# Optimization experiments

Measured on AMD Instinct MI355X. Metric: run time of the kernel, lower is better.

Reference implementation:

```python
import jax, jax.numpy as jnp
import numpy as np

N_HEADS = 16
HEAD = 64
HID = 1024
WIN = 256
LN_EPS = 1e-5


def _ln(x, g, b):
    m = jnp.mean(x, axis=-1, keepdims=True)
    v = jnp.mean((x - m) ** 2, axis=-1, keepdims=True)
    return (x - m) * jax.lax.rsqrt(v + LN_EPS) * g + b


def _window_shift(x):
    return jnp.concatenate([jnp.zeros_like(x[:, :WIN]), x[:, :-WIN]], axis=1)


def _additive_attn(x, vec, mask_add):
    B, S, _ = x.shape
    # per-head logits: (x * vec) summed within each head, scaled
    attn = (x * vec).reshape(B, S, N_HEADS, HEAD).sum(-1) / (HEAD ** 0.5)
    attn = jnp.exp(attn + mask_add)[..., None]          # [B,S,H,1]
    xh = x.reshape(B, S, N_HEADS, HEAD)
    s = jnp.cumsum(attn * xh, axis=1)
    s = s - _window_shift(s)                             # windowed cumsum of attn*x
    z = jnp.cumsum(attn, axis=1)
    z = z - _window_shift(z)                             # windowed cumsum of attn
    return (s / z).reshape(B, S, HID)


def setup_inputs():
    key = jax.random.key(0)
    ks = jax.random.split(key, 7)
    B, S = 4, 4096
    w = lambda k: (jax.random.normal(k, (HID, HID)) * 0.02).astype(jnp.float32)
    return {
        "hidden_states": jax.random.normal(ks[0], (B, S, HID), dtype=jnp.float32),
        "attention_mask": jnp.ones((B, S), dtype=jnp.float32),
        "Wq": w(ks[1]), "Wk": w(ks[2]), "Wv": w(ks[3]), "Wp": w(ks[4]),
        "query_attn": (jax.random.normal(ks[5], (HID,)) * 0.02).astype(jnp.float32),
        "key_attn": (jax.random.normal(ks[6], (HID,)) * 0.02).astype(jnp.float32),
        "ln1_g": jnp.ones((HID,), jnp.float32), "ln1_b": jnp.zeros((HID,), jnp.float32),
        "ln2_g": jnp.ones((HID,), jnp.float32), "ln2_b": jnp.zeros((HID,), jnp.float32),
    }


def reference(hidden_states, attention_mask, Wq, Wk, Wv, Wp, query_attn, key_attn,
              ln1_g, ln1_b, ln2_g, ln2_b):
    h = _ln(hidden_states, ln1_g, ln1_b)
    query = h @ Wq.T
    keys = h @ Wk.T
    values = h @ Wv.T
    mask_add = ((1.0 - attention_mask) * -10000.0)[:, :, None]  # [B,S,1]
    pooled_q = _additive_attn(query, query_attn, mask_add)
    pooled_q = pooled_q @ Wp.T                                  # (dropout is identity in eval)
    residual = h + pooled_q * keys
    mixed = _ln(residual, ln2_g, ln2_b)
    pooled_k = _additive_attn(mixed, key_attn, mask_add)
    return residual + pooled_k * values
```

## Files before the change

### kernel.cpp

```cpp
#include <hip/hip_runtime.h>
#include <hip/hip_bf16.h>

#define HID 1024
#define NH 16
#define HEAD 64
#define WIN 256
#define SEQ 4096
#define BATCH 4
#define NROWS (BATCH * SEQ)
#define LN_EPS 1e-5f

typedef unsigned short u16;
typedef __bf16 bf16x8 __attribute__((ext_vector_type(8)));
typedef float f32x4 __attribute__((ext_vector_type(4)));

static __device__ inline float bfu(u16 u) {
    union { unsigned int i; float f; } x;
    x.i = ((unsigned int)u) << 16;
    return x.f;
}

static __device__ inline u16 f2bf(float f) {
    union { float f; unsigned int i; } x;
    x.f = f;
    unsigned int lsb = (x.i >> 16) & 1u;
    x.i += 0x7fffu + lsb;
    return (u16)(x.i >> 16);
}

__global__ __launch_bounds__(256) void ln1_conv(
    const float* __restrict__ x, const float* __restrict__ g,
    const float* __restrict__ b, u16* __restrict__ out,
    const float* __restrict__ wq, const float* __restrict__ wk,
    const float* __restrict__ wv, const float* __restrict__ wp,
    u16* __restrict__ wo)
{
    __shared__ float red[8];
    int t = threadIdx.x;
    if (blockIdx.x >= NROWS) {
        int i = (blockIdx.x - NROWS) * 256 + t;
        const int n = 1024 * 1024;
        wo[i]         = f2bf(wq[i]);
        wo[n + i]     = f2bf(wk[i]);
        wo[2 * n + i] = f2bf(wv[i]);
        wo[3 * n + i] = f2bf(wp[i]);
        return;
    }
    int row = blockIdx.x;
    float4 v = ((const float4*)(x + (size_t)row * HID))[t];
    float s  = v.x + v.y + v.z + v.w;
    float ss = v.x * v.x + v.y * v.y + v.z * v.z + v.w * v.w;
    #pragma unroll
    for (int off = 32; off; off >>= 1) { s += __shfl_down(s, off); ss += __shfl_down(ss, off); }
    int wave = t >> 6, lane = t & 63;
    if (lane == 0) { red[wave] = s; red[4 + wave] = ss; }
    __syncthreads();
    float S  = red[0] + red[1] + red[2] + red[3];
    float SS = red[4] + red[5] + red[6] + red[7];
    float mean = S * (1.f / HID);
    float var  = SS * (1.f / HID) - mean * mean;
    float inv  = rsqrtf(var + LN_EPS);
    float4 gv = ((const float4*)g)[t];
    float4 bv = ((const float4*)b)[t];
    ushort4 o;
    o.x = f2bf((v.x - mean) * inv * gv.x + bv.x);
    o.y = f2bf((v.y - mean) * inv * gv.y + bv.y);
    o.z = f2bf((v.z - mean) * inv * gv.z + bv.z);
    o.w = f2bf((v.w - mean) * inv * gv.w + bv.w);
    ((ushort4*)(out + (size_t)row * HID))[t] = o;
}

#define GLDS(gp, lp) __builtin_amdgcn_global_load_lds( \
    (const __attribute__((address_space(1))) void*)(gp), \
    (__attribute__((address_space(3))) void*)(lp), 16, 0, 0)

__global__ __launch_bounds__(512, 2) void gemm256(
    const u16* __restrict__ A, const u16* __restrict__ W,
    u16* __restrict__ C, int K, int ldc, int ntiles)
{
    __shared__ __align__(16) u16 sA[2][256 * 64];
    __shared__ __align__(16) u16 sB[2][256 * 64];

    const int tid = threadIdx.x;
    const int wave = tid >> 6, lane = tid & 63;
    const int wr = wave >> 2, wc = wave & 3;

    const int rp = tid >> 3;
    const int rowA = (rp < 32 ? rp : rp + 96);
    const int colE = (((tid & 7) * 16) ^ ((rp & 7) << 4)) >> 1;
    const int c0 = ((lane >> 4) * 16) ^ ((lane & 7) << 4);
    const int li = lane & 15;

    const int nk = K >> 6;

    int a = blockIdx.x;
    int wgl = a >> 3;
    int bm = (a & 7) * 8 + (wgl & 7);
    int bn = wgl >> 3;
    const u16* gA = A + (size_t)(bm * 256 + rowA) * K + colE;
    const u16* gB = W + (size_t)(bn * 256 + rp) * K + colE;
    #pragma unroll
    for (int w = 0; w < 4; ++w) GLDS(gB + (size_t)w * 64 * K, &sB[0][w * 4096 + tid * 8]);
    #pragma unroll
    for (int p = 0; p < 4; ++p) GLDS(gA + (size_t)p * 32 * K, &sA[0][p * 4096 + tid * 8]);

    while (true) {
        f32x4 acc[8][4];
        #pragma unroll
        for (int m = 0; m < 8; ++m)
            #pragma unroll
            for (int n = 0; n < 4; ++n) {
                f32x4 z = {0.f, 0.f, 0.f, 0.f};
                acc[m][n] = z;
            }

        for (int kt = 0; kt < nk; ++kt) {
            const int b = kt & 1;
            const u16* rA = sA[b];
            const u16* rB = sB[b];
            u16* dA = sA[b ^ 1];
            u16* dB = sB[b ^ 1];
            const bool pf = (kt + 1 < nk);

            if (pf) {
                const size_t ko = (size_t)(kt + 1) * 64;
                #pragma unroll
                for (int w = 0; w < 4; ++w)
                    GLDS(gB + (size_t)w * 64 * K + ko, &dB[w * 4096 + tid * 8]);
                #pragma unroll
                for (int p = 0; p < 4; ++p)
                    GLDS(gA + (size_t)p * 32 * K + ko, &dA[p * 4096 + tid * 8]);
                asm volatile("s_waitcnt vmcnt(8)" ::: "memory");
            } else {
                asm volatile("s_waitcnt vmcnt(0)" ::: "memory");
            }
            __builtin_amdgcn_sched_barrier(0);
            __builtin_amdgcn_s_barrier();
            __builtin_amdgcn_sched_barrier(0);

            bf16x8 bF0[4], bF1[4], aF0[8], aF1[8];
            #pragma unroll
            for (int n = 0; n < 4; ++n)
                bF0[n] = *(const bf16x8*)&rB[wc * 4096 + (n * 16 + li) * 64 + (c0 >> 1)];
            #pragma unroll
            for (int mf = 0; mf < 8; ++mf)
                aF0[mf] = *(const bf16x8*)&rA[(mf >> 1) * 4096 +
                    (wr * 32 + (mf & 1) * 16 + li) * 64 + (c0 >> 1)];
            __builtin_amdgcn_s_setprio(1);
            #pragma unroll
            for (int mf = 0; mf < 8; ++mf)
                #pragma unroll
                for (int n = 0; n < 4; ++n)
                    acc[mf][n] = __builtin_amdgcn_mfma_f32_16x16x32_bf16(
                        aF0[mf], bF0[n], acc[mf][n], 0, 0, 0);
            #pragma unroll
            for (int n = 0; n < 4; ++n)
                bF1[n] = *(const bf16x8*)&rB[wc * 4096 + (n * 16 + li) * 64 + ((c0 ^ 64) >> 1)];
            #pragma unroll
            for (int mf = 0; mf < 8; ++mf)
                aF1[mf] = *(const bf16x8*)&rA[(mf >> 1) * 4096 +
                    (wr * 32 + (mf & 1) * 16 + li) * 64 + ((c0 ^ 64) >> 1)];
            #pragma unroll
            for (int mf = 0; mf < 8; ++mf)
                #pragma unroll
                for (int n = 0; n < 4; ++n)
                    acc[mf][n] = __builtin_amdgcn_mfma_f32_16x16x32_bf16(
                        aF1[mf], bF1[n], acc[mf][n], 0, 0, 0);
            __builtin_amdgcn_s_setprio(0);
            __builtin_amdgcn_sched_barrier(0);
            __builtin_amdgcn_s_barrier();
            __builtin_amdgcn_sched_barrier(0);
        }

        const int bmC = bm, bnC = bn;
        a += gridDim.x;
        const bool more = (a < ntiles);
        if (more) {
            wgl = a >> 3; bm = (a & 7) * 8 + (wgl & 7); bn = wgl >> 3;
            gA = A + (size_t)(bm * 256 + rowA) * K + colE;
            gB = W + (size_t)(bn * 256 + rp) * K + colE;
            #pragma unroll
            for (int w = 0; w < 4; ++w) GLDS(gB + (size_t)w * 64 * K, &sB[0][w * 4096 + tid * 8]);
            #pragma unroll
            for (int p = 0; p < 4; ++p) GLDS(gA + (size_t)p * 32 * K, &sA[0][p * 4096 + tid * 8]);
        }

        #pragma unroll
        for (int mf = 0; mf < 8; ++mf) {
            int row0 = bmC * 256 + wr * 128 + mf * 16 + ((lane >> 4) << 2);
            #pragma unroll
            for (int n = 0; n < 4; ++n) {
                int col = bnC * 256 + wc * 64 + n * 16 + li;
                #pragma unroll
                for (int r = 0; r < 4; ++r)
                    C[(size_t)(row0 + r) * ldc + col] = f2bf(acc[mf][n][r]);
            }
        }
        if (!more) break;
    }
}

__global__ __launch_bounds__(256) void logits_kernel(
    const u16* __restrict__ x, int xstride,
    const float* __restrict__ vec, const float* __restrict__ mask,
    float* __restrict__ aw)
{
    int h = blockIdx.y, b = blockIdx.z;
    int s = blockIdx.x * 256 + threadIdx.x;
    __shared__ float vl[HEAD];
    if (threadIdx.x < HEAD) vl[threadIdx.x] = vec[h * HEAD + threadIdx.x];
    __syncthreads();
    const uint4* xr = (const uint4*)(x + ((size_t)(b * SEQ + s)) * xstride + h * HEAD);
    float dot = 0.f;
    #pragma unroll
    for (int i = 0; i < 8; ++i) {
        uint4 v = xr[i];
        const u16* p = (const u16*)&v;
        #pragma unroll
        for (int j = 0; j < 8; ++j) dot += bfu(p[j]) * vl[i * 8 + j];
    }
    float ma = (1.0f - mask[b * SEQ + s]) * -10000.0f;
    aw[((size_t)b * NH + h) * SEQ + s] = expf(dot * 0.125f + ma);
}

__global__ __launch_bounds__(512) void attn_win2(
    const u16* __restrict__ x, int xstride,
    const float* __restrict__ aw_g,
    u16* __restrict__ out_bf,
    const u16* __restrict__ resv,
    float* __restrict__ outF,
    int fused)
{
    int c = blockIdx.x, h2 = blockIdx.y, b = blockIdx.z;
    __shared__ float awl[2][2][WIN];
    __shared__ float2 sts[2][8][64];
    __shared__ float stz[2][8][2];

    int t = threadIdx.x, wave = t >> 6, lane = t & 63;
    int hh = lane >> 5;
    int coff = hh * 64 + (lane & 31) * 2;
    bool havePrev = (c > 0);

    const float* aw0 = aw_g + ((size_t)b * NH + h2 * 2) * SEQ;
    for (int i = t; i < 1024; i += 512) {
        int hd = i >> 9, cc = (i >> 8) & 1, j = i & 255;
        float v = 0.f;
        if (cc == 1) v = aw0[hd * SEQ + c * WIN + j];
        else if (havePrev) v = aw0[hd * SEQ + (c - 1) * WIN + j];
        awl[hd][cc][j] = v;
    }
    __syncthreads();

    const u16* xb = x + (size_t)b * SEQ * xstride + h2 * 128 + coff;
    int jp0 = (havePrev ? c - 1 : c) * WIN;
    int jc0 = c * WIN;
    int j0 = wave * 32;

    float s0a = 0, s0b = 0, s1a = 0, s1b = 0, z0 = 0, z1 = 0;
    #pragma unroll 8
    for (int jj = 0; jj < 32; ++jj) {
        int j = j0 + jj;
        float ap = awl[hh][0][j], ac = awl[hh][1][j];
        unsigned up = *(const unsigned*)(xb + (size_t)(jp0 + j) * xstride);
        unsigned uc = *(const unsigned*)(xb + (size_t)(jc0 + j) * xstride);
        s0a += ap * bfu(up & 0xffff); s0b += ap * bfu(up >> 16); z0 += ap;
        s1a += ac * bfu(uc & 0xffff); s1b += ac * bfu(uc >> 16); z1 += ac;
    }
    sts[0][wave][lane] = make_float2(s0a, s0b);
    sts[1][wave][lane] = make_float2(s1a, s1b);
    if ((lane & 31) == 0) { stz[0][wave][hh] = z0; stz[1][wave][hh] = z1; }
    __syncthreads();

    float cs0a = 0, cs0b = 0, cs1a = 0, cs1b = 0, cz0 = 0, cz1 = 0;
    float totsa = 0, totsb = 0, totz = 0;
    #pragma unroll
    for (int w2 = 0; w2 < 8; ++w2) {
        float2 sp = sts[0][w2][lane];
        float zp = stz[0][w2][hh];
        totsa += sp.x; totsb += sp.y; totz += zp;
        if (w2 < wave) {
            cs0a += sp.x; cs0b += sp.y; cz0 += zp;
            float2 sc = sts[1][w2][lane];
            cs1a += sc.x; cs1b += sc.y; cz1 += stz[1][w2][hh];
        }
    }

    float rpa = cs0a, rpb = cs0b, rca = cs1a, rcb = cs1b, rzp = cz0, rzc = cz1;
    size_t rowbase = (size_t)b * SEQ + jc0;
    #pragma unroll 4
    for (int jj = 0; jj < 32; ++jj) {
        int j = j0 + jj;
        float ap = awl[hh][0][j], ac = awl[hh][1][j];
        unsigned up = *(const unsigned*)(xb + (size_t)(jp0 + j) * xstride);
        unsigned uc = *(const unsigned*)(xb + (size_t)(jc0 + j) * xstride);
        rpa += ap * bfu(up & 0xffff); rpb += ap * bfu(up >> 16); rzp += ap;
        rca += ac * bfu(uc & 0xffff); rcb += ac * bfu(uc >> 16); rzc += ac;
        float inv = 1.f / (rzc + totz - rzp);
        float wva = (rca + totsa - rpa) * inv;
        float wvb = (rcb + totsb - rpb) * inv;
        if (fused) {
            size_t roff = (rowbase + j) * 3072 + h2 * 128 + coff;
            unsigned rr = *(const unsigned*)(resv + roff);
            unsigned vv = *(const unsigned*)(resv + roff + 2048);
            float2 o;
            o.x = bfu(rr & 0xffff) + wva * bfu(vv & 0xffff);
            o.y = bfu(rr >> 16)    + wvb * bfu(vv >> 16);
            *(float2*)(outF + (rowbase + j) * HID + h2 * 128 + coff) = o;
        } else {
            unsigned pk = (unsigned)f2bf(wva) | ((unsigned)f2bf(wvb) << 16);
            *(unsigned*)(out_bf + (rowbase + j) * HID + h2 * 128 + coff) = pk;
        }
    }
}

__global__ __launch_bounds__(256) void resid_ln2(
    const u16* h, u16* qkv,
    const float* __restrict__ g, const float* __restrict__ b,
    const float* __restrict__ ka, const float* __restrict__ mask,
    u16* mixed, float* __restrict__ aw2)
{
    int row = blockIdx.x;
    int t = threadIdx.x;
    ushort4 h4 = ((const ushort4*)(h + (size_t)row * HID))[t];
    ushort4 p4 = ((const ushort4*)(qkv + (size_t)row * 3072))[t];
    ushort4 k4 = ((const ushort4*)(qkv + (size_t)row * 3072 + 1024))[t];
    float r0 = bfu(h4.x) + bfu(p4.x) * bfu(k4.x);
    float r1 = bfu(h4.y) + bfu(p4.y) * bfu(k4.y);
    float r2 = bfu(h4.z) + bfu(p4.z) * bfu(k4.z);
    float r3 = bfu(h4.w) + bfu(p4.w) * bfu(k4.w);
    ushort4 rb;
    rb.x = f2bf(r0); rb.y = f2bf(r1); rb.z = f2bf(r2); rb.w = f2bf(r3);
    ((ushort4*)(qkv + (size_t)row * 3072))[t] = rb;

    float s  = r0 + r1 + r2 + r3;
    float ss = r0 * r0 + r1 * r1 + r2 * r2 + r3 * r3;
    __shared__ float red[8];
    #pragma unroll
    for (int off = 32; off; off >>= 1) { s += __shfl_down(s, off); ss += __shfl_down(ss, off); }
    int wave = t >> 6, lane = t & 63;
    if (lane == 0) { red[wave] = s; red[4 + wave] = ss; }
    __syncthreads();
    float S  = red[0] + red[1] + red[2] + red[3];
    float SS = red[4] + red[5] + red[6] + red[7];
    float mean = S * (1.f / HID);
    float var  = SS * (1.f / HID) - mean * mean;
    float inv  = rsqrtf(var + LN_EPS);
    float4 gv = ((const float4*)g)[t];
    float4 bv = ((const float4*)b)[t];
    float n0 = (r0 - mean) * inv * gv.x + bv.x;
    float n1 = (r1 - mean) * inv * gv.y + bv.y;
    float n2 = (r2 - mean) * inv * gv.z + bv.z;
    float n3 = (r3 - mean) * inv * gv.w + bv.w;
    ushort4 o;
    o.x = f2bf(n0); o.y = f2bf(n1); o.z = f2bf(n2); o.w = f2bf(n3);
    ((ushort4*)(mixed + (size_t)row * HID))[t] = o;

    float4 kv = ((const float4*)ka)[t];
    float partial = n0 * kv.x + n1 * kv.y + n2 * kv.z + n3 * kv.w;
    partial += __shfl_xor(partial, 1);
    partial += __shfl_xor(partial, 2);
    partial += __shfl_xor(partial, 4);
    partial += __shfl_xor(partial, 8);
    if ((t & 15) == 0) {
        int hh = t >> 4;
        int bb = row >> 12, sl = row & (SEQ - 1);
        float ma = (1.0f - mask[row]) * -10000.0f;
        aw2[((size_t)bb * NH + hh) * SEQ + sl] = expf(partial * 0.125f + ma);
    }
}

extern "C" void kernel_launch(void* const* d_in, const int* in_sizes, int n_in,
                              void* d_out, int out_size, void* d_ws, size_t ws_size,
                              hipStream_t stream)
{
    const float* hidden = (const float*)d_in[0];
    const float* mask   = (const float*)d_in[1];
    const float* Wq     = (const float*)d_in[2];
    const float* Wk     = (const float*)d_in[3];
    const float* Wv     = (const float*)d_in[4];
    const float* Wp     = (const float*)d_in[5];
    const float* qa     = (const float*)d_in[6];
    const float* ka     = (const float*)d_in[7];
    const float* g1     = (const float*)d_in[8];
    const float* b1     = (const float*)d_in[9];
    const float* g2     = (const float*)d_in[10];
    const float* b2     = (const float*)d_in[11];
    float* out = (float*)d_out;

    char* ws = (char*)d_ws;
    u16* wbf = (u16*)ws;       ws += (size_t)4 * 1024 * 1024 * 2;
    u16* hbf = (u16*)ws;       ws += (size_t)NROWS * HID * 2;
    u16* qkv = (u16*)ws;       ws += (size_t)NROWS * 3072 * 2;
    u16* pooled = (u16*)ws;    ws += (size_t)NROWS * HID * 2;
    float* aw1 = (float*)ws;   ws += (size_t)BATCH * NH * SEQ * 4;
    float* aw2 = (float*)ws;

    ln1_conv<<<NROWS + 4096, 256, 0, stream>>>(hidden, g1, b1, hbf, Wq, Wk, Wv, Wp, wbf);
    gemm256<<<256, 512, 0, stream>>>(hbf, wbf, qkv, HID, 3072, 768);
    logits_kernel<<<dim3(SEQ / 256, NH, BATCH), 256, 0, stream>>>(qkv, 3072, qa, mask, aw1);
    attn_win2<<<dim3(SEQ / WIN, NH / 2, BATCH), 512, 0, stream>>>(
        qkv, 3072, aw1, pooled, (const u16*)nullptr, (float*)nullptr, 0);
    gemm256<<<256, 512, 0, stream>>>(pooled, wbf + (size_t)3 * 1024 * 1024, qkv, HID, 3072, 256);
    resid_ln2<<<NROWS, 256, 0, stream>>>(hbf, qkv, g2, b2, ka, mask, hbf, aw2);
    attn_win2<<<dim3(SEQ / WIN, NH / 2, BATCH), 512, 0, stream>>>(
        hbf, HID, aw2, (u16*)nullptr, qkv, out, 1);
}
```

Measured before the change: 283.9 us.

## Replace persistent 256x256 BK64 GEMM with non-persistent 256x128 BK32 triple-buffered GEMM

The GEMM is rewritten from a persistent 256x256 tile kernel with K-step 64 and double buffering into a one-tile-per-block 256x128 kernel with K-step 32 and a three-stage LDS ring. LDS use drops from 128 KB to 72 KB per block and accumulator registers are halved, so launch bounds ask for 4 blocks per CU and the grid grows to 1536 and 512 blocks. The aim is higher occupancy and deeper prefetch to hide global-load latency. In exchange, smaller tiles reuse data less, each K step does less work per barrier, and K=1024 is now hard-coded.

```diff
diff --git a/kernel.cpp b/kernel.cpp
--- a/kernel.cpp
+++ b/kernel.cpp
@@ -74,129 +74,112 @@
     (const __attribute__((address_space(1))) void*)(gp), \
     (__attribute__((address_space(3))) void*)(lp), 16, 0, 0)
 
-__global__ __launch_bounds__(512, 2) void gemm256(
+__global__ __launch_bounds__(512, 4) void gemm_bk32(
     const u16* __restrict__ A, const u16* __restrict__ W,
-    u16* __restrict__ C, int K, int ldc, int ntiles)
-{
-    __shared__ __align__(16) u16 sA[2][256 * 64];
-    __shared__ __align__(16) u16 sB[2][256 * 64];
+    u16* __restrict__ C, int ldc)
+{
+    __shared__ __align__(16) u16 lds[3][12288];
 
     const int tid = threadIdx.x;
     const int wave = tid >> 6, lane = tid & 63;
     const int wr = wave >> 2, wc = wave & 3;
-
-    const int rp = tid >> 3;
-    const int rowA = (rp < 32 ? rp : rp + 96);
-    const int colE = (((tid & 7) * 16) ^ ((rp & 7) << 4)) >> 1;
-    const int c0 = ((lane >> 4) * 16) ^ ((lane & 7) << 4);
     const int li = lane & 15;
-
-    const int nk = K >> 6;
-
-    int a = blockIdx.x;
-    int wgl = a >> 3;
-    int bm = (a & 7) * 8 + (wgl & 7);
-    int bn = wgl >> 3;
-    const u16* gA = A + (size_t)(bm * 256 + rowA) * K + colE;
-    const u16* gB = W + (size_t)(bn * 256 + rp) * K + colE;
-    #pragma unroll
-    for (int w = 0; w < 4; ++w) GLDS(gB + (size_t)w * 64 * K, &sB[0][w * 4096 + tid * 8]);
-    #pragma unroll
-    for (int p = 0; p < 4; ++p) GLDS(gA + (size_t)p * 32 * K, &sA[0][p * 4096 + tid * 8]);
-
-    while (true) {
-        f32x4 acc[8][4];
-        #pragma unroll
-        for (int m = 0; m < 8; ++m)
+    const int kg = lane >> 4;
+    const int swz = (kg * 8) ^ ((li & 3) << 3);
+
+    const int bm = (blockIdx.x & 7) * 8 + ((blockIdx.x >> 3) & 7);
+    const int bn = blockIdx.x >> 6;
+
+    const int rp = tid >> 2;
+    const int colE = (((tid & 3) * 16) ^ ((rp & 3) << 4)) >> 1;
+    const int rowA0 = rp + (rp >= 64 ? 64 : 0);
+    const u16* gA0 = A + (size_t)(bm * 256 + rowA0) * 1024 + colE;
+    const u16* gA1 = gA0 + (size_t)64 * 1024;
+    const u16* gB  = W + (size_t)(bn * 128 + rp) * 1024 + colE;
+
+    #pragma unroll
+    for (int t = 0; t < 2; ++t) {
+        u16* d = &lds[t][0];
+        GLDS(gA0 + t * 32, d + tid * 8);
+        GLDS(gA1 + t * 32, d + 4096 + tid * 8);
+        GLDS(gB  + t * 32, d + 8192 + tid * 8);
+    }
+    asm volatile("s_waitcnt vmcnt(3)" ::: "memory");
+    __builtin_amdgcn_sched_barrier(0);
+    __builtin_amdgcn_s_barrier();
+    __builtin_amdgcn_sched_barrier(0);
+
+    f32x4 acc[8][2];
+    #pragma unroll
+    for (int m = 0; m < 8; ++m)
+        #pragma unroll
+        for (int n = 0; n < 2; ++n) {
+            f32x4 z = {0.f, 0.f, 0.f, 0.f};
+            acc[m][n] = z;
+        }
+
+    const u16* rb = &lds[0][0];
+    const u16* rn = &lds[1][0];
+    u16* wb = &lds[2][0];
+
+    for (int kt = 0; kt < 32; ++kt) {
+        bf16x8 bF[2], aFl[4];
+        #pragma unroll
+        for (int n = 0; n < 2; ++n)
+            bF[n] = *(const bf16x8*)&rb[8192 + (wc * 32 + n * 16 + li) * 32 + swz];
+        #pragma unroll
+        for (int i = 0; i < 4; ++i)
+            aFl[i] = *(const bf16x8*)&rb[(wr * 64 + i * 16 + li) * 32 + swz];
+
+        if (kt < 30) {
+            const int ko = (kt + 2) * 32;
+            GLDS(gA0 + ko, wb + tid * 8);
+            GLDS(gA1 + ko, wb + 4096 + tid * 8);
+            GLDS(gB  + ko, wb + 8192 + tid * 8);
+        }
+        if (kt < 31) {
+            if (kt < 30) asm volatile("s_waitcnt vmcnt(3)" ::: "memory");
+            else         asm volatile("s_waitcnt vmcnt(0)" ::: "memory");
+        }
+        __builtin_amdgcn_sched_barrier(0);
+        __builtin_amdgcn_s_barrier();
+        __builtin_amdgcn_sched_barrier(0);
+
+        __builtin_amdgcn_s_setprio(1);
+        #pragma unroll
+        for (int i = 0; i < 4; ++i)
             #pragma unroll
-            for (int n = 0; n < 4; ++n) {
-                f32x4 z = {0.f, 0.f, 0.f, 0.f};
-                acc[m][n] = z;
-            }
-
-        for (int kt = 0; kt < nk; ++kt) {
-            const int b = kt & 1;
-            const u16* rA = sA[b];
-            const u16* rB = sB[b];
-            u16* dA = sA[b ^ 1];
-            u16* dB = sB[b ^ 1];
-            const bool pf = (kt + 1 < nk);
-
-            if (pf) {
-                const size_t ko = (size_t)(kt + 1) * 64;
-                #pragma unroll
-                for (int w = 0; w < 4; ++w)
-                    GLDS(gB + (size_t)w * 64 * K + ko, &dB[w * 4096 + tid * 8]);
-                #pragma unroll
-                for (int p = 0; p < 4; ++p)
-                    GLDS(gA + (size_t)p * 32 * K + ko, &dA[p * 4096 + tid * 8]);
-                asm volatile("s_waitcnt vmcnt(8)" ::: "memory");
-            } else {
-                asm volatile("s_waitcnt vmcnt(0)" ::: "memory");
-            }
-            __builtin_amdgcn_sched_barrier(0);
-            __builtin_amdgcn_s_barrier();
-            __builtin_amdgcn_sched_barrier(0);
-
-            bf16x8 bF0[4], bF1[4], aF0[8], aF1[8];
+            for (int n = 0; n < 2; ++n)
+                acc[i][n] = __builtin_amdgcn_mfma_f32_16x16x32_bf16(
+                    aFl[i], bF[n], acc[i][n], 0, 0, 0);
+        bf16x8 aFh[4];
+        #pragma unroll
+        for (int i = 0; i < 4; ++i)
+            aFh[i] = *(const bf16x8*)&rb[4096 + (wr * 64 + i * 16 + li) * 32 + swz];
+        #pragma unroll
+        for (int i = 0; i < 4; ++i)
             #pragma unroll
-            for (int n = 0; n < 4; ++n)
-                bF0[n] = *(const bf16x8*)&rB[wc * 4096 + (n * 16 + li) * 64 + (c0 >> 1)];
+            for (int n = 0; n < 2; ++n)
+                acc[4 + i][n] = __builtin_amdgcn_mfma_f32_16x16x32_bf16(
+                    aFh[i], bF[n], acc[4 + i][n], 0, 0, 0);
+        __builtin_amdgcn_s_setprio(0);
+        __builtin_amdgcn_sched_barrier(0);
+        __builtin_amdgcn_s_barrier();
+        __builtin_amdgcn_sched_barrier(0);
+
+        const u16* tmp = rb; rb = rn; rn = wb; wb = (u16*)tmp;
+    }
+
+    #pragma unroll
+    for (int mf = 0; mf < 8; ++mf) {
+        int row0 = bm * 256 + wr * 128 + mf * 16 + kg * 4;
+        #pragma unroll
+        for (int n = 0; n < 2; ++n) {
+            int col = bn * 128 + wc * 32 + n * 16 + li;
             #pragma unroll
-            for (int mf = 0; mf < 8; ++mf)
-                aF0[mf] = *(const bf16x8*)&rA[(mf >> 1) * 4096 +
-                    (wr * 32 + (mf & 1) * 16 + li) * 64 + (c0 >> 1)];
-            __builtin_amdgcn_s_setprio(1);
-            #pragma unroll
-            for (int mf = 0; mf < 8; ++mf)
-                #pragma unroll
-                for (int n = 0; n < 4; ++n)
-                    acc[mf][n] = __builtin_amdgcn_mfma_f32_16x16x32_bf16(
-                        aF0[mf], bF0[n], acc[mf][n], 0, 0, 0);
-            #pragma unroll
-            for (int n = 0; n < 4; ++n)
-                bF1[n] = *(const bf16x8*)&rB[wc * 4096 + (n * 16 + li) * 64 + ((c0 ^ 64) >> 1)];
-            #pragma unroll
-            for (int mf = 0; mf < 8; ++mf)
-                aF1[mf] = *(const bf16x8*)&rA[(mf >> 1) * 4096 +
-                    (wr * 32 + (mf & 1) * 16 + li) * 64 + ((c0 ^ 64) >> 1)];
-            #pragma unroll
-            for (int mf = 0; mf < 8; ++mf)
-                #pragma unroll
-                for (int n = 0; n < 4; ++n)
-                    acc[mf][n] = __builtin_amdgcn_mfma_f32_16x16x32_bf16(
-                        aF1[mf], bF1[n], acc[mf][n], 0, 0, 0);
-            __builtin_amdgcn_s_setprio(0);
-            __builtin_amdgcn_sched_barrier(0);
-            __builtin_amdgcn_s_barrier();
-            __builtin_amdgcn_sched_barrier(0);
-        }
-
-        const int bmC = bm, bnC = bn;
-        a += gridDim.x;
-        const bool more = (a < ntiles);
-        if (more) {
-            wgl = a >> 3; bm = (a & 7) * 8 + (wgl & 7); bn = wgl >> 3;
-            gA = A + (size_t)(bm * 256 + rowA) * K + colE;
-            gB = W + (size_t)(bn * 256 + rp) * K + colE;
-            #pragma unroll
-            for (int w = 0; w < 4; ++w) GLDS(gB + (size_t)w * 64 * K, &sB[0][w * 4096 + tid * 8]);
-            #pragma unroll
-            for (int p = 0; p < 4; ++p) GLDS(gA + (size_t)p * 32 * K, &sA[0][p * 4096 + tid * 8]);
-        }
-
-        #pragma unroll
-        for (int mf = 0; mf < 8; ++mf) {
-            int row0 = bmC * 256 + wr * 128 + mf * 16 + ((lane >> 4) << 2);
-            #pragma unroll
-            for (int n = 0; n < 4; ++n) {
-                int col = bnC * 256 + wc * 64 + n * 16 + li;
-                #pragma unroll
-                for (int r = 0; r < 4; ++r)
-                    C[(size_t)(row0 + r) * ldc + col] = f2bf(acc[mf][n][r]);
-            }
-        }
-        if (!more) break;
+            for (int r = 0; r < 4; ++r)
+                C[(size_t)(row0 + r) * ldc + col] = f2bf(acc[mf][n][r]);
+        }
     }
 }
 
@@ -396,11 +379,11 @@
     float* aw2 = (float*)ws;
 
     ln1_conv<<<NROWS + 4096, 256, 0, stream>>>(hidden, g1, b1, hbf, Wq, Wk, Wv, Wp, wbf);
-    gemm256<<<256, 512, 0, stream>>>(hbf, wbf, qkv, HID, 3072, 768);
+    gemm_bk32<<<1536, 512, 0, stream>>>(hbf, wbf, qkv, 3072);
     logits_kernel<<<dim3(SEQ / 256, NH, BATCH), 256, 0, stream>>>(qkv, 3072, qa, mask, aw1);
     attn_win2<<<dim3(SEQ / WIN, NH / 2, BATCH), 512, 0, stream>>>(
         qkv, 3072, aw1, pooled, (const u16*)nullptr, (float*)nullptr, 0);
-    gemm256<<<256, 512, 0, stream>>>(pooled, wbf + (size_t)3 * 1024 * 1024, qkv, HID, 3072, 256);
+    gemm_bk32<<<512, 512, 0, stream>>>(pooled, wbf + (size_t)3 * 1024 * 1024, qkv, 3072);
     resid_ln2<<<NROWS, 256, 0, stream>>>(hbf, qkv, g2, b2, ka, mask, hbf, aw2);
     attn_win2<<<dim3(SEQ / WIN, NH / 2, BATCH), 512, 0, stream>>>(
         hbf, HID, aw2, (u16*)nullptr, qkv, out, 1);
```

Measured after the change: 288.5 us. About the same (+1.6%).
